# Performance work log

Measured on AMD Instinct MI355X. Metric: run time of the kernel, lower is better.

Reference implementation:

```python
import jax, jax.numpy as jnp
import numpy as np

N_HEADS = 8
N_LANDMARKS = 64
NEWTON_ITERS = 6


def _iterative_inv(mat):
    # mat: [B,H,L,L]; Newton-Schulz approximate inverse, 6 iterations
    L = mat.shape[-1]
    fro = jnp.sqrt(jnp.sum(mat * mat, axis=(-2, -1), keepdims=True))
    fro = jnp.maximum(fro, 1e-6)
    z = jnp.swapaxes(mat, -2, -1) / (fro * fro)
    for _ in range(NEWTON_ITERS):
        z = 2.0 * z - z @ mat @ z
    return z


def setup_inputs() -> dict:
    key = jax.random.key(0)
    ks = jax.random.split(key, 5)
    B, N, C = 4, 8192, 512
    s = 1.0 / np.sqrt(C)
    return {
        "x": jax.random.normal(ks[0], (B, N, C), jnp.float32),
        "Wqkv": jax.random.normal(ks[1], (3 * C, C), jnp.float32) * s,
        "bqkv": jax.random.normal(ks[2], (3 * C,), jnp.float32) * 0.01,
        "Wproj": jax.random.normal(ks[3], (C, C), jnp.float32) * s,
        "bproj": jax.random.normal(ks[4], (C,), jnp.float32) * 0.01,
    }


def reference(x, Wqkv, bqkv, Wproj, bproj):
    B, N, C = x.shape
    H = N_HEADS
    hd = C // H
    scale = hd ** (-0.5)
    n_lm = N_LANDMARKS

    qkv = x @ Wqkv.T + bqkv                       # [B,N,3C]
    qkv = qkv.reshape(B, N, 3, H, hd).transpose(2, 0, 3, 1, 4)  # [3,B,H,N,hd]
    q, k, v = qkv[0], qkv[1], qkv[2]

    if N <= n_lm:
        attn = jax.nn.softmax(q @ jnp.swapaxes(k, -2, -1) * scale, axis=-1)
        out = attn @ v
    else:
        stride = max(N // n_lm, 1)
        lm_idx = jnp.arange(0, N, stride)[:n_lm]
        q_lm = q[:, :, lm_idx]                    # [B,H,L,hd]
        k_lm = k[:, :, lm_idx]
        kernel_1 = jax.nn.softmax(q @ jnp.swapaxes(k_lm, -2, -1) * scale, axis=-1)   # [B,H,N,L]
        kernel_2 = jax.nn.softmax(q_lm @ jnp.swapaxes(k_lm, -2, -1) * scale, axis=-1)  # [B,H,L,L]
        kernel_3 = jax.nn.softmax(q_lm @ jnp.swapaxes(k, -2, -1) * scale, axis=-1)   # [B,H,L,N]
        kernel_2_inv = _iterative_inv(kernel_2)
        out = kernel_1 @ (kernel_2_inv @ (kernel_3 @ v))  # [B,H,N,hd]

    out = jnp.swapaxes(out, 1, 2).reshape(B, N, C)
    return out @ Wproj.T + bproj
```

## Files before the change

kernel.cpp:

```cpp
#include <hip/hip_runtime.h>

typedef unsigned short u16;
typedef unsigned int u32;

typedef __bf16 v8bf __attribute__((ext_vector_type(8)));
typedef float v4f __attribute__((ext_vector_type(4)));
typedef u16 v8u __attribute__((ext_vector_type(8)));

#define N_TOK 8192
#define CDIM 512
#define HEADS 8
#define HD 64
#define LM 64
#define LSTRIDE 128
#define BHN 32
#define NCHUNK 16
#define SCALE 0.125f

__device__ __forceinline__ float b2f(u16 u) { return __uint_as_float(((u32)u) << 16); }
__device__ __forceinline__ u16 f2bf(float f) {
  u32 u = __float_as_uint(f);
  u += 0x7fffu + ((u >> 16) & 1u);
  return (u16)(u >> 16);
}
__device__ __forceinline__ u32 pk2bf(float a, float b) {
  return (u32)f2bf(a) | ((u32)f2bf(b) << 16);
}

__device__ __forceinline__ void gl_lds16(const u16* g, u16* l) {
  __builtin_amdgcn_global_load_lds(
      (const __attribute__((address_space(1))) u32*)g,
      (__attribute__((address_space(3))) u32*)l, 16, 0, 0);
}

__global__ __launch_bounds__(256) void cast_bf16(const float* __restrict__ src,
                                                 u16* __restrict__ dst, int n8) {
  int i = blockIdx.x * 256 + threadIdx.x;
  if (i >= n8) return;
  const float4* s = (const float4*)src;
  float4 a = s[(size_t)i * 2], b = s[(size_t)i * 2 + 1];
  uint4 o;
  o.x = (u32)f2bf(a.x) | ((u32)f2bf(a.y) << 16);
  o.y = (u32)f2bf(a.z) | ((u32)f2bf(a.w) << 16);
  o.z = (u32)f2bf(b.x) | ((u32)f2bf(b.y) << 16);
  o.w = (u32)f2bf(b.z) | ((u32)f2bf(b.w) << 16);
  *(uint4*)(dst + (size_t)i * 8) = o;
}

template <int MODE>
__global__ __launch_bounds__(256) void gemm_bt(const u16* __restrict__ A,
                                               const u16* __restrict__ Bm,
                                               const float* __restrict__ bias,
                                               u16* __restrict__ qo,
                                               u16* __restrict__ ko,
                                               u16* __restrict__ vo,
                                               float* __restrict__ outp) {
  __shared__ __align__(16) u16 As[128 * 32];
  __shared__ __align__(16) u16 Bs[128 * 32];
  const int K = 512;
  const int m0 = blockIdx.x * 128;
  const int n0 = blockIdx.y * 128;
  const int t = threadIdx.x;
  const int lane = t & 63, w = t >> 6;
  const int wm = w >> 1, wn = w & 1;
  const int quad = lane >> 4, lrow = lane & 15;

  v4f acc[4][4];
#pragma unroll
  for (int i = 0; i < 4; ++i)
#pragma unroll
    for (int j = 0; j < 4; ++j)
#pragma unroll
      for (int r = 0; r < 4; ++r) acc[i][j][r] = 0.f;

  for (int kt = 0; kt < K; kt += 32) {
    __syncthreads();
#pragma unroll
    for (int p = 0; p < 2; ++p) {
      int ci = p * 256 + t;
      int r = ci >> 2, s = ci & 3;
      int cs = (s ^ (r >> 1)) & 3;
      gl_lds16(A + (size_t)(m0 + r) * K + kt + cs * 8, &As[ci * 8]);
      gl_lds16(Bm + (size_t)(n0 + r) * K + kt + cs * 8, &Bs[ci * 8]);
    }
    __syncthreads();
    v8bf af[4], bf[4];
#pragma unroll
    for (int ti = 0; ti < 4; ++ti) {
      int row = wm * 64 + ti * 16 + lrow;
      af[ti] = *(const v8bf*)&As[row * 32 + ((quad ^ (row >> 1)) & 3) * 8];
    }
#pragma unroll
    for (int tj = 0; tj < 4; ++tj) {
      int row = wn * 64 + tj * 16 + lrow;
      bf[tj] = *(const v8bf*)&Bs[row * 32 + ((quad ^ (row >> 1)) & 3) * 8];
    }
#pragma unroll
    for (int ti = 0; ti < 4; ++ti)
#pragma unroll
      for (int tj = 0; tj < 4; ++tj)
        acc[ti][tj] = __builtin_amdgcn_mfma_f32_16x16x32_bf16(af[ti], bf[tj], acc[ti][tj], 0, 0, 0);
  }

#pragma unroll
  for (int ti = 0; ti < 4; ++ti) {
#pragma unroll
    for (int tj = 0; tj < 4; ++tj) {
      int gn = n0 + wn * 64 + tj * 16 + lrow;
      float bv = bias[gn];
#pragma unroll
      for (int r = 0; r < 4; ++r) {
        int gm = m0 + wm * 64 + ti * 16 + quad * 4 + r;
        float val = acc[ti][tj][r] + bv;
        if (MODE == 0) {
          int tt = gn >> 9;
          int h = (gn >> 6) & 7;
          int d = gn & 63;
          int b = gm >> 13;
          int n = gm & 8191;
          size_t di = ((size_t)(b * HEADS + h) * N_TOK + n) * HD + d;
          u16* dst = (tt == 0) ? qo : (tt == 1) ? ko : vo;
          dst[di] = f2bf(val);
        } else {
          outp[(size_t)gm * CDIM + gn] = val;
        }
      }
    }
  }
}

__global__ __launch_bounds__(256) void fpart(const u16* __restrict__ qb,
                                             const u16* __restrict__ kb,
                                             const u16* __restrict__ vb,
                                             float* __restrict__ Fp,
                                             float* __restrict__ Mc,
                                             float* __restrict__ Sc) {
  __shared__ __align__(16) char smem[4 * 64 * 40 * 2 * 2];
  __shared__ float msh[4][64], ssh[4][64];
  const int jc = blockIdx.x, bh = blockIdx.y;
  const int t = threadIdx.x;
  const int lane = t & 63, w = t >> 6;
  const int col = lane & 15, quad = lane >> 4;
  const int jq = lane & 7, dh = lane >> 3;

  u16* Pw = (u16*)smem + w * (64 * 40);
  u16* vT = (u16*)smem + 4 * (64 * 40) + w * (64 * 40);
  float* Fbuf = (float*)smem;

  v8bf qf[4][2];
#pragma unroll
  for (int it = 0; it < 4; ++it)
#pragma unroll
    for (int kh = 0; kh < 2; ++kh)
      qf[it][kh] = *(const v8bf*)(qb + ((size_t)bh * N_TOK + (size_t)(it * 16 + col) * LSTRIDE) * HD + kh * 32 + quad * 8);

  float mw[4], sw[4];
  v4f facc[4][4];
#pragma unroll
  for (int it = 0; it < 4; ++it) { mw[it] = -3.0e38f; sw[it] = 0.f; }
#pragma unroll
  for (int dt = 0; dt < 4; ++dt)
#pragma unroll
    for (int it = 0; it < 4; ++it)
#pragma unroll
      for (int r = 0; r < 4; ++r) facc[dt][it][r] = 0.f;

  for (int st = 0; st < 4; ++st) {
    const int j0 = jc * 512 + w * 128 + st * 32;

    v8bf kf[2][2];
#pragma unroll
    for (int jt = 0; jt < 2; ++jt)
#pragma unroll
      for (int kh = 0; kh < 2; ++kh)
        kf[jt][kh] = *(const v8bf*)(kb + ((size_t)bh * N_TOK + j0 + jt * 16 + col) * HD + kh * 32 + quad * 8);

    v8u r0 = *(const v8u*)(vb + ((size_t)bh * N_TOK + j0 + jq * 4 + 0) * HD + dh * 8);
    v8u r1 = *(const v8u*)(vb + ((size_t)bh * N_TOK + j0 + jq * 4 + 1) * HD + dh * 8);
    v8u r2 = *(const v8u*)(vb + ((size_t)bh * N_TOK + j0 + jq * 4 + 2) * HD + dh * 8);
    v8u r3 = *(const v8u*)(vb + ((size_t)bh * N_TOK + j0 + jq * 4 + 3) * HD + dh * 8);
#pragma unroll
    for (int e = 0; e < 8; ++e) {
      uint2 pk;
      pk.x = (u32)r0[e] | ((u32)r1[e] << 16);
      pk.y = (u32)r2[e] | ((u32)r3[e] << 16);
      *(uint2*)&vT[(dh * 8 + e) * 40 + jq * 4] = pk;
    }

    v4f sacc[2][4];
#pragma unroll
    for (int jt = 0; jt < 2; ++jt)
#pragma unroll
      for (int it = 0; it < 4; ++it) {
#pragma unroll
        for (int r = 0; r < 4; ++r) sacc[jt][it][r] = 0.f;
#pragma unroll
        for (int kh = 0; kh < 2; ++kh)
          sacc[jt][it] = __builtin_amdgcn_mfma_f32_16x16x32_bf16(kf[jt][kh], qf[it][kh], sacc[jt][it], 0, 0, 0);
      }

#pragma unroll
    for (int it = 0; it < 4; ++it) {
      float mloc = -3.0e38f;
#pragma unroll
      for (int jt = 0; jt < 2; ++jt)
#pragma unroll
        for (int r = 0; r < 4; ++r) {
          float s = sacc[jt][it][r] * SCALE;
          sacc[jt][it][r] = s;
          mloc = fmaxf(mloc, s);
        }
      mloc = fmaxf(mloc, __shfl_xor(mloc, 16));
      mloc = fmaxf(mloc, __shfl_xor(mloc, 32));
      float mnew = fmaxf(mw[it], mloc);
      float alpha = __expf(mw[it] - mnew);
      mw[it] = mnew;
      float rs = 0.f;
#pragma unroll
      for (int jt = 0; jt < 2; ++jt)
#pragma unroll
        for (int r = 0; r < 4; ++r) {
          float p = __expf(sacc[jt][it][r] - mnew);
          sacc[jt][it][r] = p;
          rs += p;
        }
      rs += __shfl_xor(rs, 16);
      rs += __shfl_xor(rs, 32);
      sw[it] = sw[it] * alpha + rs;
#pragma unroll
      for (int jt = 0; jt < 2; ++jt) {
        uint2 pk;
        pk.x = pk2bf(sacc[jt][it][0], sacc[jt][it][1]);
        pk.y = pk2bf(sacc[jt][it][2], sacc[jt][it][3]);
        *(uint2*)&Pw[(it * 16 + col) * 40 + jt * 16 + quad * 4] = pk;
      }
#pragma unroll
      for (int dt = 0; dt < 4; ++dt)
#pragma unroll
        for (int r = 0; r < 4; ++r) facc[dt][it][r] *= alpha;
    }

    v8bf vfr[4], pfr[4];
#pragma unroll
    for (int dt = 0; dt < 4; ++dt)
      vfr[dt] = *(const v8bf*)&vT[(dt * 16 + col) * 40 + quad * 8];
#pragma unroll
    for (int it = 0; it < 4; ++it)
      pfr[it] = *(const v8bf*)&Pw[(it * 16 + col) * 40 + quad * 8];
#pragma unroll
    for (int dt = 0; dt < 4; ++dt)
#pragma unroll
      for (int it = 0; it < 4; ++it)
        facc[dt][it] = __builtin_amdgcn_mfma_f32_16x16x32_bf16(vfr[dt], pfr[it], facc[dt][it], 0, 0, 0);
  }

  if (quad == 0) {
#pragma unroll
    for (int it = 0; it < 4; ++it) {
      msh[w][it * 16 + col] = mw[it];
      ssh[w][it * 16 + col] = sw[it];
    }
  }
  __syncthreads();

  const size_t cb = (size_t)(bh * NCHUNK + jc) * 64;
  float scl[4];
#pragma unroll
  for (int it = 0; it < 4; ++it) {
    int i = it * 16 + col;
    float m0 = msh[0][i], m1 = msh[1][i], m2 = msh[2][i], m3 = msh[3][i];
    float M = fmaxf(fmaxf(m0, m1), fmaxf(m2, m3));
    float e0 = __expf(m0 - M), e1 = __expf(m1 - M);
    float e2 = __expf(m2 - M), e3 = __expf(m3 - M);
    float Stot = e0 * ssh[0][i] + e1 * ssh[1][i] + e2 * ssh[2][i] + e3 * ssh[3][i];
    scl[it] = (w == 0) ? e0 : (w == 1) ? e1 : (w == 2) ? e2 : e3;
    if (w == 0 && quad == 0) {
      Mc[cb + i] = M;
      Sc[cb + i] = Stot;
    }
  }

  for (int wv = 0; wv < 4; ++wv) {
    if (w == wv) {
#pragma unroll
      for (int it = 0; it < 4; ++it)
#pragma unroll
        for (int dt = 0; dt < 4; ++dt) {
          float* dst = &Fbuf[(it * 16 + col) * 76 + dt * 16 + quad * 4];
          float4 v;
          v.x = facc[dt][it][0] * scl[it];
          v.y = facc[dt][it][1] * scl[it];
          v.z = facc[dt][it][2] * scl[it];
          v.w = facc[dt][it][3] * scl[it];
          if (wv == 0) {
            *(float4*)dst = v;
          } else {
            float4 o = *(float4*)dst;
            o.x += v.x; o.y += v.y; o.z += v.z; o.w += v.w;
            *(float4*)dst = o;
          }
        }
    }
    __syncthreads();
  }

  size_t base = (size_t)(bh * NCHUNK + jc) * 4096;
#pragma unroll
  for (int p = 0; p < 16; ++p) {
    int idx = p * 256 + t;
    Fp[base + idx] = Fbuf[(idx >> 6) * 76 + (idx & 63)];
  }
}

__global__ __launch_bounds__(256) void newton_t(const u16* __restrict__ qb,
                                                const u16* __restrict__ kb,
                                                const float* __restrict__ Fp,
                                                const float* __restrict__ Mc,
                                                const float* __restrict__ Sc,
                                                u16* __restrict__ Tt) {
  __shared__ float Ms[4096];
  __shared__ float Z0s[4096];
  __shared__ float Ws[4096];
  __shared__ float Xs[4096];
  const int bh = blockIdx.x;
  const int t = threadIdx.x;
  const int lane = t & 63, w = t >> 6;
  const int ti = t >> 4, tj = t & 15;

#pragma unroll
  for (int p = 0; p < 16; ++p) {
    int idx = p * 256 + t;
    int i = idx >> 6, d = idx & 63;
    Ws[idx] = b2f(qb[((size_t)bh * N_TOK + i * LSTRIDE) * HD + d]);
    Xs[d * 64 + i] = b2f(kb[((size_t)bh * N_TOK + i * LSTRIDE) * HD + d]);
  }
  __syncthreads();

  {
    float a2[4][4];
#pragma unroll
    for (int a = 0; a < 4; ++a)
#pragma unroll
      for (int b = 0; b < 4; ++b) a2[a][b] = 0.f;
    for (int d = 0; d < 64; ++d) {
      float qa[4], kv[4];
#pragma unroll
      for (int a = 0; a < 4; ++a) qa[a] = Ws[(ti * 4 + a) * 64 + d];
#pragma unroll
      for (int b = 0; b < 4; ++b) kv[b] = Xs[d * 64 + tj * 4 + b];
#pragma unroll
      for (int a = 0; a < 4; ++a)
#pragma unroll
        for (int b = 0; b < 4; ++b) a2[a][b] += qa[a] * kv[b];
    }
    __syncthreads();
#pragma unroll
    for (int a = 0; a < 4; ++a)
#pragma unroll
      for (int b = 0; b < 4; ++b) Ms[(ti * 4 + a) * 64 + tj * 4 + b] = a2[a][b] * SCALE;
  }
  __syncthreads();

  for (int rr = 0; rr < 16; ++rr) {
    int i = w * 16 + rr;
    float vv = Ms[i * 64 + lane];
    float m = vv;
#pragma unroll
    for (int off = 32; off; off >>= 1) m = fmaxf(m, __shfl_xor(m, off));
    float e = expf(vv - m);
    float s = e;
#pragma unroll
    for (int off = 32; off; off >>= 1) s += __shfl_xor(s, off);
    Ms[i * 64 + lane] = e / s;
  }
  __syncthreads();

  float loc = 0.f;
#pragma unroll
  for (int p = 0; p < 16; ++p) {
    float v = Ms[p * 256 + t];
    loc += v * v;
  }
#pragma unroll
  for (int off = 32; off; off >>= 1) loc += __shfl_xor(loc, off);
  if (lane == 0) Z0s[w] = loc;
  __syncthreads();
  float fro = fmaxf(sqrtf(Z0s[0] + Z0s[1] + Z0s[2] + Z0s[3]), 1e-6f);
  float invden = 1.0f / (fro * fro);
  __syncthreads();

#pragma unroll
  for (int p = 0; p < 16; ++p) {
    int idx = p * 256 + t;
    int i = idx >> 6, j = idx & 63;
    Z0s[j * 64 + i] = Ms[idx] * invden;
  }
  __syncthreads();

  float* Z = Z0s;
  float* Zn = Xs;
  for (int it = 0; it < 6; ++it) {
    {
      float a2[4][4];
#pragma unroll
      for (int a = 0; a < 4; ++a)
#pragma unroll
        for (int b = 0; b < 4; ++b) a2[a][b] = 0.f;
      for (int tt = 0; tt < 64; ++tt) {
        float za[4], mb[4];
#pragma unroll
        for (int a = 0; a < 4; ++a) za[a] = Z[(ti * 4 + a) * 64 + tt];
#pragma unroll
        for (int b = 0; b < 4; ++b) mb[b] = Ms[tt * 64 + tj * 4 + b];
#pragma unroll
        for (int a = 0; a < 4; ++a)
#pragma unroll
          for (int b = 0; b < 4; ++b) a2[a][b] += za[a] * mb[b];
      }
#pragma unroll
      for (int a = 0; a < 4; ++a)
#pragma unroll
        for (int b = 0; b < 4; ++b) Ws[(ti * 4 + a) * 64 + tj * 4 + b] = a2[a][b];
    }
    __syncthreads();
    {
      float a2[4][4];
#pragma unroll
      for (int a = 0; a < 4; ++a)
#pragma unroll
        for (int b = 0; b < 4; ++b) a2[a][b] = 0.f;
      for (int tt = 0; tt < 64; ++tt) {
        float wa[4], zb[4];
#pragma unroll
        for (int a = 0; a < 4; ++a) wa[a] = Ws[(ti * 4 + a) * 64 + tt];
#pragma unroll
        for (int b = 0; b < 4; ++b) zb[b] = Z[tt * 64 + tj * 4 + b];
#pragma unroll
        for (int a = 0; a < 4; ++a)
#pragma unroll
          for (int b = 0; b < 4; ++b) a2[a][b] += wa[a] * zb[b];
      }
#pragma unroll
      for (int a = 0; a < 4; ++a)
#pragma unroll
        for (int b = 0; b < 4; ++b)
          Zn[(ti * 4 + a) * 64 + tj * 4 + b] =
              2.f * Z[(ti * 4 + a) * 64 + tj * 4 + b] - a2[a][b];
    }
    __syncthreads();
    float* tmp = Z; Z = Zn; Zn = tmp;
  }

  float* wts = Ms;
  if (t < 64) {
    float M = -3.0e38f;
#pragma unroll
    for (int jc = 0; jc < NCHUNK; ++jc)
      M = fmaxf(M, Mc[(bh * NCHUNK + jc) * 64 + t]);
    float S = 0.f;
#pragma unroll
    for (int jc = 0; jc < NCHUNK; ++jc)
      S += expf(Mc[(bh * NCHUNK + jc) * 64 + t] - M) * Sc[(bh * NCHUNK + jc) * 64 + t];
    float invS = 1.0f / S;
#pragma unroll
    for (int jc = 0; jc < NCHUNK; ++jc)
      wts[jc * 64 + t] = expf(Mc[(bh * NCHUNK + jc) * 64 + t] - M) * invS;
  }
  __syncthreads();

#pragma unroll
  for (int p = 0; p < 16; ++p) {
    int idx = p * 256 + t;
    int i = idx >> 6;
    float sum = 0.f;
#pragma unroll
    for (int jc = 0; jc < NCHUNK; ++jc)
      sum += wts[jc * 64 + i] * Fp[(size_t)(bh * NCHUNK + jc) * 4096 + idx];
    Ws[idx] = sum;
  }
  __syncthreads();

  {
    float a2[4][4];
#pragma unroll
    for (int a = 0; a < 4; ++a)
#pragma unroll
      for (int b = 0; b < 4; ++b) a2[a][b] = 0.f;
    for (int tt = 0; tt < 64; ++tt) {
      float za[4], fb[4];
#pragma unroll
      for (int a = 0; a < 4; ++a) za[a] = Z[(ti * 4 + a) * 64 + tt];
#pragma unroll
      for (int b = 0; b < 4; ++b) fb[b] = Ws[tt * 64 + tj * 4 + b];
#pragma unroll
      for (int a = 0; a < 4; ++a)
#pragma unroll
        for (int b = 0; b < 4; ++b) a2[a][b] += za[a] * fb[b];
    }
#pragma unroll
    for (int a = 0; a < 4; ++a)
#pragma unroll
      for (int b = 0; b < 4; ++b)
        Tt[(size_t)bh * 4096 + (size_t)(tj * 4 + b) * 64 + (ti * 4 + a)] = f2bf(a2[a][b]);
  }
}

__global__ __launch_bounds__(256) void attn_out_k(const u16* __restrict__ qb,
                                                  const u16* __restrict__ kb,
                                                  const u16* __restrict__ Tt,
                                                  u16* __restrict__ ao) {
  __shared__ __align__(16) u16 Pl[4][1024];
  const int bh = blockIdx.y;
  const int b = bh >> 3, h = bh & 7;
  const int t = threadIdx.x;
  const int lane = t & 63, w = t >> 6;
  const int col = lane & 15, quad = lane >> 4;
  const int rot = (col & 7) * 8;

  v8bf kfr[4][2], tfr[4][2];
#pragma unroll
  for (int tj = 0; tj < 4; ++tj)
#pragma unroll
    for (int kh = 0; kh < 2; ++kh)
      kfr[tj][kh] = *(const v8bf*)(kb + ((size_t)bh * N_TOK + (size_t)(tj * 16 + col) * LSTRIDE) * HD + kh * 32 + quad * 8);
#pragma unroll
  for (int td = 0; td < 4; ++td)
#pragma unroll
    for (int jh = 0; jh < 2; ++jh)
      tfr[td][jh] = *(const v8bf*)(Tt + (size_t)bh * 4096 + (size_t)(td * 16 + col) * 64 + jh * 32 + quad * 8);

  u16* Pw = &Pl[w][0];

  for (int tile = 0; tile < 4; ++tile) {
    const int n0 = blockIdx.x * 256 + w * 64 + tile * 16;
    v8bf qf[2];
#pragma unroll
    for (int kh = 0; kh < 2; ++kh)
      qf[kh] = *(const v8bf*)(qb + ((size_t)bh * N_TOK + n0 + col) * HD + kh * 32 + quad * 8);

    v4f S[4];
#pragma unroll
    for (int tj = 0; tj < 4; ++tj) {
#pragma unroll
      for (int r = 0; r < 4; ++r) S[tj][r] = 0.f;
#pragma unroll
      for (int kh = 0; kh < 2; ++kh)
        S[tj] = __builtin_amdgcn_mfma_f32_16x16x32_bf16(kfr[tj][kh], qf[kh], S[tj], 0, 0, 0);
    }

    float mx = -3.0e38f;
#pragma unroll
    for (int tj = 0; tj < 4; ++tj)
#pragma unroll
      for (int r = 0; r < 4; ++r) {
        S[tj][r] *= SCALE;
        mx = fmaxf(mx, S[tj][r]);
      }
    mx = fmaxf(mx, __shfl_xor(mx, 16));
    mx = fmaxf(mx, __shfl_xor(mx, 32));
    float sum = 0.f;
#pragma unroll
    for (int tj = 0; tj < 4; ++tj)
#pragma unroll
      for (int r = 0; r < 4; ++r) {
        S[tj][r] = __expf(S[tj][r] - mx);
        sum += S[tj][r];
      }
    sum += __shfl_xor(sum, 16);
    sum += __shfl_xor(sum, 32);
    float inv = 1.0f / sum;

#pragma unroll
    for (int tj = 0; tj < 4; ++tj) {
      u32 lo = (u32)f2bf(S[tj][0] * inv) | ((u32)f2bf(S[tj][1] * inv) << 16);
      u32 hi = (u32)f2bf(S[tj][2] * inv) | ((u32)f2bf(S[tj][3] * inv) << 16);
      uint2 pk = {lo, hi};
      *(uint2*)&Pw[col * 64 + ((tj * 16 + quad * 4 + rot) & 63)] = pk;
    }
    v8bf pf[2];
#pragma unroll
    for (int jh = 0; jh < 2; ++jh)
      pf[jh] = *(const v8bf*)&Pw[col * 64 + ((jh * 32 + quad * 8 + rot) & 63)];

    v4f O[4];
#pragma unroll
    for (int td = 0; td < 4; ++td) {
#pragma unroll
      for (int r = 0; r < 4; ++r) O[td][r] = 0.f;
#pragma unroll
      for (int jh = 0; jh < 2; ++jh)
        O[td] = __builtin_amdgcn_mfma_f32_16x16x32_bf16(pf[jh], tfr[td][jh], O[td], 0, 0, 0);
    }
#pragma unroll
    for (int td = 0; td < 4; ++td)
#pragma unroll
      for (int r = 0; r < 4; ++r) {
        int n = n0 + quad * 4 + r;
        ao[((size_t)(b * N_TOK + n)) * CDIM + h * HD + td * 16 + col] = f2bf(O[td][r]);
      }
  }
}

__global__ void ws_too_small_sentinel(float* out) {
  if (threadIdx.x == 0 && blockIdx.x == 0) out[0] = 1.0f;
}

static constexpr size_t SZ_QKV = (size_t)BHN * N_TOK * HD * 2;
static constexpr size_t OFF_Q = 0;
static constexpr size_t OFF_K = OFF_Q + SZ_QKV;
static constexpr size_t OFF_V = OFF_K + SZ_QKV;
static constexpr size_t OFF_FP = OFF_V + SZ_QKV;
static constexpr size_t SZ_FP = (size_t)BHN * NCHUNK * 4096 * 4;
static constexpr size_t OFF_MC = OFF_FP + SZ_FP;
static constexpr size_t SZ_MS = (size_t)BHN * NCHUNK * 64 * 4;
static constexpr size_t OFF_SC = OFF_MC + SZ_MS;
static constexpr size_t OFF_T = OFF_SC + SZ_MS;
static constexpr size_t OFF_WQ = OFF_T + (size_t)BHN * 4096 * 2;
static constexpr size_t OFF_WP = OFF_WQ + (size_t)3 * CDIM * CDIM * 2;
static constexpr size_t OFF_END = OFF_WP + (size_t)CDIM * CDIM * 2;

extern "C" void kernel_launch(void* const* d_in, const int* in_sizes, int n_in,
                              void* d_out, int out_size, void* d_ws, size_t ws_size,
                              hipStream_t stream) {
  const float* x = (const float*)d_in[0];
  const float* Wqkv = (const float*)d_in[1];
  const float* bqkv = (const float*)d_in[2];
  const float* Wproj = (const float*)d_in[3];
  const float* bproj = (const float*)d_in[4];
  float* out = (float*)d_out;
  char* ws = (char*)d_ws;
  if (ws_size < OFF_END) {
    ws_too_small_sentinel<<<1, 64, 0, stream>>>(out);
    return;
  }

  u16* qb = (u16*)(ws + OFF_Q);
  u16* kb = (u16*)(ws + OFF_K);
  u16* vb = (u16*)(ws + OFF_V);
  float* Fp = (float*)(ws + OFF_FP);
  float* Mc = (float*)(ws + OFF_MC);
  float* Sc = (float*)(ws + OFF_SC);
  u16* Tt = (u16*)(ws + OFF_T);
  u16* Wqb = (u16*)(ws + OFF_WQ);
  u16* Wpb = (u16*)(ws + OFF_WP);
  u16* attn = (u16*)(ws + OFF_V);
  u16* xb = (u16*)d_out;

  cast_bf16<<<8192, 256, 0, stream>>>(x, xb, 2097152);
  cast_bf16<<<384, 256, 0, stream>>>(Wqkv, Wqb, 98304);
  cast_bf16<<<128, 256, 0, stream>>>(Wproj, Wpb, 32768);
  gemm_bt<0><<<dim3(256, 12), 256, 0, stream>>>(xb, Wqb, bqkv, qb, kb, vb, nullptr);
  fpart<<<dim3(NCHUNK, BHN), 256, 0, stream>>>(qb, kb, vb, Fp, Mc, Sc);
  newton_t<<<dim3(BHN), 256, 0, stream>>>(qb, kb, Fp, Mc, Sc, Tt);
  attn_out_k<<<dim3(32, BHN), 256, 0, stream>>>(qb, kb, Tt, attn);
  gemm_bt<1><<<dim3(256, 4), 256, 0, stream>>>(attn, Wpb, bproj, nullptr, nullptr, nullptr, out);
}
```

Before: 313.7 us.

## Run Newton-Schulz inverse on MFMA with split bf16 hi/lo precision

Rewrites the newton_t kernel so the 64x64 matrix products (landmark scores, the six Newton iterations, and the final Z·F product) run on bf16 MFMA instructions instead of scalar fp32 FMAs in LDS. Each fp32 operand is split into bf16 high and low parts, and three MFMAs per product approximate fp32 accuracy. Operands are stored in XOR-swizzled LDS tiles, and Z is kept in registers across iterations. This cuts the scalar ALU cost of this serial per-head kernel, at the price of extra conversion work and a small precision loss in the iterative inverse.

```diff
diff --git a/kernel.cpp b/kernel.cpp
--- a/kernel.cpp
+++ b/kernel.cpp
@@ -31,6 +31,15 @@
   __builtin_amdgcn_global_load_lds(
       (const __attribute__((address_space(1))) u32*)g,
       (__attribute__((address_space(3))) u32*)l, 16, 0, 0);
+}
+
+__device__ __forceinline__ void wr_hl(u16* __restrict__ h, u16* __restrict__ l,
+                                      int row, int col, float v) {
+  u16 hi = f2bf(v);
+  u16 lo = f2bf(v - b2f(hi));
+  int a = row * 64 + (((col >> 3) ^ (row & 7)) << 3) + (col & 7);
+  h[a] = hi;
+  l[a] = lo;
 }
 
 __global__ __launch_bounds__(256) void cast_bf16(const float* __restrict__ src,
@@ -312,197 +321,199 @@
   }
 }
 
+__device__ __forceinline__ void mm_hl(const u16* __restrict__ Ah,
+                                      const u16* __restrict__ Al,
+                                      const u16* __restrict__ Bh,
+                                      const u16* __restrict__ Bl,
+                                      int Ra, int quad, int lrow, v4f out[4]) {
+  v8bf ah[2], al[2];
+#pragma unroll
+  for (int kk = 0; kk < 2; ++kk) {
+    int c8 = (((kk * 4 + quad) ^ (Ra & 7)) * 8);
+    ah[kk] = *(const v8bf*)&Ah[Ra * 64 + c8];
+    al[kk] = *(const v8bf*)&Al[Ra * 64 + c8];
+  }
+#pragma unroll
+  for (int nt = 0; nt < 4; ++nt) {
+    int Rb = nt * 16 + lrow;
+#pragma unroll
+    for (int kk = 0; kk < 2; ++kk) {
+      int c8 = (((kk * 4 + quad) ^ (Rb & 7)) * 8);
+      v8bf bh = *(const v8bf*)&Bh[Rb * 64 + c8];
+      v8bf bl = *(const v8bf*)&Bl[Rb * 64 + c8];
+      out[nt] = __builtin_amdgcn_mfma_f32_16x16x32_bf16(ah[kk], bh, out[nt], 0, 0, 0);
+      out[nt] = __builtin_amdgcn_mfma_f32_16x16x32_bf16(ah[kk], bl, out[nt], 0, 0, 0);
+      out[nt] = __builtin_amdgcn_mfma_f32_16x16x32_bf16(al[kk], bh, out[nt], 0, 0, 0);
+    }
+  }
+}
+
 __global__ __launch_bounds__(256) void newton_t(const u16* __restrict__ qb,
                                                 const u16* __restrict__ kb,
                                                 const float* __restrict__ Fp,
                                                 const float* __restrict__ Mc,
                                                 const float* __restrict__ Sc,
                                                 u16* __restrict__ Tt) {
-  __shared__ float Ms[4096];
-  __shared__ float Z0s[4096];
-  __shared__ float Ws[4096];
-  __shared__ float Xs[4096];
+  __shared__ float Sf[4096];
+  __shared__ float red[4];
+  __shared__ __align__(16) u16 mTh[4096], mTl[4096];
+  __shared__ __align__(16) u16 zh_[4096], zl_[4096];
+  __shared__ __align__(16) u16 zTh[4096], zTl[4096];
+  __shared__ __align__(16) u16 wh_[4096], wl_[4096];
   const int bh = blockIdx.x;
-  const int t = threadIdx.x;
-  const int lane = t & 63, w = t >> 6;
-  const int ti = t >> 4, tj = t & 15;
-
-#pragma unroll
+  const int t = threadIdx.x, lane = t & 63, w = t >> 6;
+  const int quad = lane >> 4, lrow = lane & 15;
+  const int Ra = w * 16 + lrow;
+  const int Rd = w * 16 + quad * 4;
+
+  {
+    v8bf qf[2], kf[4][2];
+#pragma unroll
+    for (int kk = 0; kk < 2; ++kk)
+      qf[kk] = *(const v8bf*)(qb + ((size_t)bh * N_TOK + (size_t)Ra * LSTRIDE) * HD + kk * 32 + quad * 8);
+#pragma unroll
+    for (int nt = 0; nt < 4; ++nt)
+#pragma unroll
+      for (int kk = 0; kk < 2; ++kk)
+        kf[nt][kk] = *(const v8bf*)(kb + ((size_t)bh * N_TOK + (size_t)(nt * 16 + lrow) * LSTRIDE) * HD + kk * 32 + quad * 8);
+    v4f sa[4];
+#pragma unroll
+    for (int nt = 0; nt < 4; ++nt) {
+#pragma unroll
+      for (int r = 0; r < 4; ++r) sa[nt][r] = 0.f;
+#pragma unroll
+      for (int kk = 0; kk < 2; ++kk)
+        sa[nt] = __builtin_amdgcn_mfma_f32_16x16x32_bf16(qf[kk], kf[nt][kk], sa[nt], 0, 0, 0);
+    }
+#pragma unroll
+    for (int nt = 0; nt < 4; ++nt)
+#pragma unroll
+      for (int r = 0; r < 4; ++r)
+        Sf[(Rd + r) * 64 + nt * 16 + lrow] = sa[nt][r] * SCALE;
+  }
+  __syncthreads();
+
+  for (int rr = 0; rr < 16; ++rr) {
+    int i = w * 16 + rr;
+    float vv = Sf[i * 64 + lane];
+    float m = vv;
+#pragma unroll
+    for (int off = 32; off; off >>= 1) m = fmaxf(m, __shfl_xor(m, off));
+    float e = expf(vv - m);
+    float s = e;
+#pragma unroll
+    for (int off = 32; off; off >>= 1) s += __shfl_xor(s, off);
+    Sf[i * 64 + lane] = e / s;
+  }
+  __syncthreads();
+
+  float loc = 0.f;
+#pragma unroll
+  for (int p = 0; p < 16; ++p) {
+    float v = Sf[p * 256 + t];
+    loc += v * v;
+  }
+#pragma unroll
+  for (int off = 32; off; off >>= 1) loc += __shfl_xor(loc, off);
+  if (lane == 0) red[w] = loc;
+  __syncthreads();
+  float fro = fmaxf(sqrtf(red[0] + red[1] + red[2] + red[3]), 1e-6f);
+  float inv = 1.0f / (fro * fro);
+
+  for (int p = 0; p < 16; ++p) {
+    int idx = p * 256 + t;
+    int r = idx >> 6, c = idx & 63;
+    float Mrc = Sf[r * 64 + c];
+    float Mcr = Sf[c * 64 + r];
+    wr_hl(mTh, mTl, r, c, Mcr);
+    wr_hl(zh_, zl_, r, c, Mcr * inv);
+    wr_hl(zTh, zTl, r, c, Mrc * inv);
+  }
+  float zr[4][4];
+#pragma unroll
+  for (int nt = 0; nt < 4; ++nt)
+#pragma unroll
+    for (int r = 0; r < 4; ++r)
+      zr[nt][r] = Sf[(nt * 16 + lrow) * 64 + Rd + r] * inv;
+  __syncthreads();
+
+  for (int it = 0; it < 6; ++it) {
+    v4f aw[4];
+#pragma unroll
+    for (int nt = 0; nt < 4; ++nt)
+#pragma unroll
+      for (int r = 0; r < 4; ++r) aw[nt][r] = 0.f;
+    mm_hl(zh_, zl_, mTh, mTl, Ra, quad, lrow, aw);
+#pragma unroll
+    for (int nt = 0; nt < 4; ++nt)
+#pragma unroll
+      for (int r = 0; r < 4; ++r)
+        wr_hl(wh_, wl_, Rd + r, nt * 16 + lrow, aw[nt][r]);
+    __syncthreads();
+
+    v4f ap[4];
+#pragma unroll
+    for (int nt = 0; nt < 4; ++nt)
+#pragma unroll
+      for (int r = 0; r < 4; ++r) ap[nt][r] = 0.f;
+    mm_hl(wh_, wl_, zTh, zTl, Ra, quad, lrow, ap);
+    float znr[4][4];
+#pragma unroll
+    for (int nt = 0; nt < 4; ++nt)
+#pragma unroll
+      for (int r = 0; r < 4; ++r)
+        znr[nt][r] = 2.f * zr[nt][r] - ap[nt][r];
+    __syncthreads();
+
+#pragma unroll
+    for (int nt = 0; nt < 4; ++nt)
+#pragma unroll
+      for (int r = 0; r < 4; ++r) {
+        zr[nt][r] = znr[nt][r];
+        wr_hl(zh_, zl_, Rd + r, nt * 16 + lrow, znr[nt][r]);
+        wr_hl(zTh, zTl, nt * 16 + lrow, Rd + r, znr[nt][r]);
+      }
+    __syncthreads();
+  }
+
+  if (t < 64) {
+    float M = -3.0e38f;
+#pragma unroll
+    for (int jc = 0; jc < NCHUNK; ++jc)
+      M = fmaxf(M, Mc[(bh * NCHUNK + jc) * 64 + t]);
+    float S = 0.f;
+#pragma unroll
+    for (int jc = 0; jc < NCHUNK; ++jc)
+      S += expf(Mc[(bh * NCHUNK + jc) * 64 + t] - M) * Sc[(bh * NCHUNK + jc) * 64 + t];
+    float invS = 1.0f / S;
+#pragma unroll
+    for (int jc = 0; jc < NCHUNK; ++jc)
+      Sf[jc * 64 + t] = expf(Mc[(bh * NCHUNK + jc) * 64 + t] - M) * invS;
+  }
+  __syncthreads();
+
   for (int p = 0; p < 16; ++p) {
     int idx = p * 256 + t;
     int i = idx >> 6, d = idx & 63;
-    Ws[idx] = b2f(qb[((size_t)bh * N_TOK + i * LSTRIDE) * HD + d]);
-    Xs[d * 64 + i] = b2f(kb[((size_t)bh * N_TOK + i * LSTRIDE) * HD + d]);
+    float sum = 0.f;
+#pragma unroll
+    for (int jc = 0; jc < NCHUNK; ++jc)
+      sum += Sf[jc * 64 + i] * Fp[(size_t)(bh * NCHUNK + jc) * 4096 + idx];
+    wr_hl(wh_, wl_, d, i, sum);
   }
   __syncthreads();
 
-  {
-    float a2[4][4];
-#pragma unroll
-    for (int a = 0; a < 4; ++a)
-#pragma unroll
-      for (int b = 0; b < 4; ++b) a2[a][b] = 0.f;
-    for (int d = 0; d < 64; ++d) {
-      float qa[4], kv[4];
-#pragma unroll
-      for (int a = 0; a < 4; ++a) qa[a] = Ws[(ti * 4 + a) * 64 + d];
-#pragma unroll
-      for (int b = 0; b < 4; ++b) kv[b] = Xs[d * 64 + tj * 4 + b];
-#pragma unroll
-      for (int a = 0; a < 4; ++a)
-#pragma unroll
-        for (int b = 0; b < 4; ++b) a2[a][b] += qa[a] * kv[b];
-    }
-    __syncthreads();
-#pragma unroll
-    for (int a = 0; a < 4; ++a)
-#pragma unroll
-      for (int b = 0; b < 4; ++b) Ms[(ti * 4 + a) * 64 + tj * 4 + b] = a2[a][b] * SCALE;
-  }
-  __syncthreads();
-
-  for (int rr = 0; rr < 16; ++rr) {
-    int i = w * 16 + rr;
-    float vv = Ms[i * 64 + lane];
-    float m = vv;
-#pragma unroll
-    for (int off = 32; off; off >>= 1) m = fmaxf(m, __shfl_xor(m, off));
-    float e = expf(vv - m);
-    float s = e;
-#pragma unroll
-    for (int off = 32; off; off >>= 1) s += __shfl_xor(s, off);
-    Ms[i * 64 + lane] = e / s;
-  }
-  __syncthreads();
-
-  float loc = 0.f;
-#pragma unroll
-  for (int p = 0; p < 16; ++p) {
-    float v = Ms[p * 256 + t];
-    loc += v * v;
-  }
-#pragma unroll
-  for (int off = 32; off; off >>= 1) loc += __shfl_xor(loc, off);
-  if (lane == 0) Z0s[w] = loc;
-  __syncthreads();
-  float fro = fmaxf(sqrtf(Z0s[0] + Z0s[1] + Z0s[2] + Z0s[3]), 1e-6f);
-  float invden = 1.0f / (fro * fro);
-  __syncthreads();
-
-#pragma unroll
-  for (int p = 0; p < 16; ++p) {
-    int idx = p * 256 + t;
-    int i = idx >> 6, j = idx & 63;
-    Z0s[j * 64 + i] = Ms[idx] * invden;
-  }
-  __syncthreads();
-
-  float* Z = Z0s;
-  float* Zn = Xs;
-  for (int it = 0; it < 6; ++it) {
-    {
-      float a2[4][4];
-#pragma unroll
-      for (int a = 0; a < 4; ++a)
-#pragma unroll
-        for (int b = 0; b < 4; ++b) a2[a][b] = 0.f;
-      for (int tt = 0; tt < 64; ++tt) {
-        float za[4], mb[4];
-#pragma unroll
-        for (int a = 0; a < 4; ++a) za[a] = Z[(ti * 4 + a) * 64 + tt];
-#pragma unroll
-        for (int b = 0; b < 4; ++b) mb[b] = Ms[tt * 64 + tj * 4 + b];
-#pragma unroll
-        for (int a = 0; a < 4; ++a)
-#pragma unroll
-          for (int b = 0; b < 4; ++b) a2[a][b] += za[a] * mb[b];
-      }
-#pragma unroll
-      for (int a = 0; a < 4; ++a)
-#pragma unroll
-        for (int b = 0; b < 4; ++b) Ws[(ti * 4 + a) * 64 + tj * 4 + b] = a2[a][b];
-    }
-    __syncthreads();
-    {
-      float a2[4][4];
-#pragma unroll
-      for (int a = 0; a < 4; ++a)
-#pragma unroll
-        for (int b = 0; b < 4; ++b) a2[a][b] = 0.f;
-      for (int tt = 0; tt < 64; ++tt) {
-        float wa[4], zb[4];
-#pragma unroll
-        for (int a = 0; a < 4; ++a) wa[a] = Ws[(ti * 4 + a) * 64 + tt];
-#pragma unroll
-        for (int b = 0; b < 4; ++b) zb[b] = Z[tt * 64 + tj * 4 + b];
-#pragma unroll
-        for (int a = 0; a < 4; ++a)
-#pragma unroll
-          for (int b = 0; b < 4; ++b) a2[a][b] += wa[a] * zb[b];
-      }
-#pragma unroll
-      for (int a = 0; a < 4; ++a)
-#pragma unroll
-        for (int b = 0; b < 4; ++b)
-          Zn[(ti * 4 + a) * 64 + tj * 4 + b] =
-              2.f * Z[(ti * 4 + a) * 64 + tj * 4 + b] - a2[a][b];
-    }
-    __syncthreads();
-    float* tmp = Z; Z = Zn; Zn = tmp;
-  }
-
-  float* wts = Ms;
-  if (t < 64) {
-    float M = -3.0e38f;
-#pragma unroll
-    for (int jc = 0; jc < NCHUNK; ++jc)
-      M = fmaxf(M, Mc[(bh * NCHUNK + jc) * 64 + t]);
-    float S = 0.f;
-#pragma unroll
-    for (int jc = 0; jc < NCHUNK; ++jc)
-      S += expf(Mc[(bh * NCHUNK + jc) * 64 + t] - M) * Sc[(bh * NCHUNK + jc) * 64 + t];
-    float invS = 1.0f / S;
-#pragma unroll
-    for (int jc = 0; jc < NCHUNK; ++jc)
-      wts[jc * 64 + t] = expf(Mc[(bh * NCHUNK + jc) * 64 + t] - M) * invS;
-  }
-  __syncthreads();
-
-#pragma unroll
-  for (int p = 0; p < 16; ++p) {
-    int idx = p * 256 + t;
-    int i = idx >> 6;
-    float sum = 0.f;
-#pragma unroll
-    for (int jc = 0; jc < NCHUNK; ++jc)
-      sum += wts[jc * 64 + i] * Fp[(size_t)(bh * NCHUNK + jc) * 4096 + idx];
-    Ws[idx] = sum;
-  }
-  __syncthreads();
-
-  {
-    float a2[4][4];
-#pragma unroll
-    for (int a = 0; a < 4; ++a)
-#pragma unroll
-      for (int b = 0; b < 4; ++b) a2[a][b] = 0.f;
-    for (int tt = 0; tt < 64; ++tt) {
-      float za[4], fb[4];
-#pragma unroll
-      for (int a = 0; a < 4; ++a) za[a] = Z[(ti * 4 + a) * 64 + tt];
-#pragma unroll
-      for (int b = 0; b < 4; ++b) fb[b] = Ws[tt * 64 + tj * 4 + b];
-#pragma unroll
-      for (int a = 0; a < 4; ++a)
-#pragma unroll
-        for (int b = 0; b < 4; ++b) a2[a][b] += za[a] * fb[b];
-    }
-#pragma unroll
-    for (int a = 0; a < 4; ++a)
-#pragma unroll
-      for (int b = 0; b < 4; ++b)
-        Tt[(size_t)bh * 4096 + (size_t)(tj * 4 + b) * 64 + (ti * 4 + a)] = f2bf(a2[a][b]);
-  }
+  v4f at[4];
+#pragma unroll
+  for (int nt = 0; nt < 4; ++nt)
+#pragma unroll
+    for (int r = 0; r < 4; ++r) at[nt][r] = 0.f;
+  mm_hl(zh_, zl_, wh_, wl_, Ra, quad, lrow, at);
+#pragma unroll
+  for (int nt = 0; nt < 4; ++nt)
+#pragma unroll
+    for (int r = 0; r < 4; ++r)
+      Tt[(size_t)bh * 4096 + (size_t)(nt * 16 + lrow) * 64 + (Rd + r)] = f2bf(at[nt][r]);
 }
 
 __global__ __launch_bounds__(256) void attn_out_k(const u16* __restrict__ qb,
```

Result: faster. 298.7 us (-4.8%).
